# Optimization experiments

Measured on AMD Instinct MI355X. Metric: run time of the kernel, lower is better.

The kernel has to match this reference:

```python
import jax, jax.numpy as jnp
import numpy as np

DIM = 3072
KV_DIM = 2048
HEADS = 16
DIM_HEAD = 128
INNER = HEADS * DIM_HEAD  # 2048
EPS = 1e-5


def layer_norm(x, g, b):
    mu = jnp.mean(x, axis=-1, keepdims=True)
    var = jnp.var(x, axis=-1, keepdims=True)
    return (x - mu) * jax.lax.rsqrt(var + EPS) * g + b


def setup_inputs() -> dict:
    key = jax.random.key(0)
    ks = jax.random.split(key, 8)
    b, n1, n2 = 2, 2048, 2048
    x = jax.random.normal(ks[0], (b, n1, KV_DIM), dtype=jnp.float32)
    latents = jax.random.normal(ks[1], (b, n2, DIM), dtype=jnp.float32)
    w_q = jax.random.normal(ks[2], (DIM, INNER), dtype=jnp.float32) / np.sqrt(DIM)
    w_kv = jax.random.normal(ks[3], (KV_DIM, 2 * INNER), dtype=jnp.float32) / np.sqrt(KV_DIM)
    w_out = jax.random.normal(ks[4], (INNER, DIM), dtype=jnp.float32) / np.sqrt(INNER)
    ln1_g = jnp.ones((KV_DIM,), jnp.float32)
    ln1_b = jnp.zeros((KV_DIM,), jnp.float32)
    ln2_g = jnp.ones((DIM,), jnp.float32)
    ln2_b = jnp.zeros((DIM,), jnp.float32)
    return {"x": x, "latents": latents, "w_q": w_q, "w_kv": w_kv,
            "w_out": w_out, "ln1_g": ln1_g, "ln1_b": ln1_b,
            "ln2_g": ln2_g, "ln2_b": ln2_b}


def reference(x, latents, w_q, w_kv, w_out, ln1_g, ln1_b, ln2_g, ln2_b):
    b, n2, _ = latents.shape
    xn = layer_norm(x, ln1_g, ln1_b)            # (b, n1, kv_dim)
    ln = layer_norm(latents, ln2_g, ln2_b)      # (b, n2, dim)
    q = ln @ w_q                                # (b, n2, inner)
    kv = xn @ w_kv                              # (b, n1, 2*inner)
    k, v = jnp.split(kv, 2, axis=-1)
    # (b, h, n, d)
    def split_heads(t):
        bs, n, _ = t.shape
        return t.reshape(bs, n, HEADS, DIM_HEAD).transpose(0, 2, 1, 3)
    q, k, v = split_heads(q), split_heads(k), split_heads(v)
    scale = 1.0 / np.sqrt(np.sqrt(DIM_HEAD)).astype(np.float32)
    w = jnp.einsum('bhqd,bhkd->bhqk', q * scale, k * scale)
    w = jax.nn.softmax(w.astype(jnp.float32), axis=-1).astype(q.dtype)
    out = jnp.einsum('bhqk,bhkd->bhqd', w, v)
    out = out.transpose(0, 2, 1, 3).reshape(b, n2, INNER)
    return out @ w_out
```

## Files before the change

### kernel.cpp

```cpp
#include <hip/hip_runtime.h>
#include <type_traits>


using u16 = unsigned short;
using u32 = unsigned int;
typedef __attribute__((ext_vector_type(8))) short short8;
typedef __attribute__((ext_vector_type(4))) float floatx4;

typedef __attribute__((address_space(1))) const unsigned int gu32;
typedef __attribute__((address_space(3))) unsigned int lu32;

__device__ __forceinline__ void gld16(void* lds, const void* g) {
  __builtin_amdgcn_global_load_lds((gu32*)g, (lu32*)lds, 16, 0, 0);
}

__device__ inline u16 f2bf(float f) {
  u32 u = __float_as_uint(f);
  u32 r = (u + 0x7FFFu + ((u >> 16) & 1u)) >> 16;
  return (u16)r;
}

template <int L>
__global__ __launch_bounds__(256) void ln_cast(const float* __restrict__ in,
                                               const float* __restrict__ gw,
                                               const float* __restrict__ bw,
                                               u16* __restrict__ out) {
  constexpr int C4 = L / 1024;
  const int row = blockIdx.x;
  const int t = threadIdx.x;
  const float* rp = in + (size_t)row * L;
  float4 v[C4];
  float s = 0.f, ss = 0.f;
#pragma unroll
  for (int c = 0; c < C4; ++c) {
    v[c] = *(const float4*)(rp + (c * 256 + t) * 4);
    s += v[c].x + v[c].y + v[c].z + v[c].w;
    ss += v[c].x * v[c].x + v[c].y * v[c].y + v[c].z * v[c].z + v[c].w * v[c].w;
  }
#pragma unroll
  for (int off = 32; off > 0; off >>= 1) {
    s += __shfl_down(s, off);
    ss += __shfl_down(ss, off);
  }
  __shared__ float red[8];
  const int wave = t >> 6, lane = t & 63;
  if (lane == 0) { red[wave] = s; red[4 + wave] = ss; }
  __syncthreads();
  const float tot = red[0] + red[1] + red[2] + red[3];
  const float tss = red[4] + red[5] + red[6] + red[7];
  const float mu = tot * (1.f / L);
  const float rstd = rsqrtf(tss * (1.f / L) - mu * mu + 1e-5f);
  u16* op = out + (size_t)row * L;
#pragma unroll
  for (int c = 0; c < C4; ++c) {
    const int base = (c * 256 + t) * 4;
    float4 gv = *(const float4*)(gw + base);
    float4 bv = *(const float4*)(bw + base);
    u32 p0 = (u32)f2bf((v[c].x - mu) * rstd * gv.x + bv.x) |
             ((u32)f2bf((v[c].y - mu) * rstd * gv.y + bv.y) << 16);
    u32 p1 = (u32)f2bf((v[c].z - mu) * rstd * gv.z + bv.z) |
             ((u32)f2bf((v[c].w - mu) * rstd * gv.w + bv.w) << 16);
    uint2 pk; pk.x = p0; pk.y = p1;
    *(uint2*)(op + base) = pk;
  }
}

__global__ __launch_bounds__(256) void transpose_cast(const float* __restrict__ in,
                                                      u16* __restrict__ out,
                                                      int R, int C) {
  __shared__ u16 tile[32][33];
  const int c0 = blockIdx.x * 32, r0 = blockIdx.y * 32;
  const int x = threadIdx.x, y = threadIdx.y;
#pragma unroll
  for (int j = 0; j < 4; ++j)
    tile[y + 8 * j][x] = f2bf(in[(size_t)(r0 + y + 8 * j) * C + c0 + x]);
  __syncthreads();
#pragma unroll
  for (int j = 0; j < 4; ++j)
    out[(size_t)(c0 + y + 8 * j) * R + r0 + x] = tile[x][y + 8 * j];
}

__global__ __launch_bounds__(256) void transpose_v(const u16* __restrict__ kvb,
                                                   u16* __restrict__ vT) {
  __shared__ u16 tile[32][33];
  const int bh = blockIdx.z, b = bh >> 4, h = bh & 15;
  const u16* src = kvb + (size_t)b * 2048 * 4096 + 2048 + h * 128;
  u16* dst = vT + (size_t)bh * 128 * 2048;
  const int d0 = blockIdx.x * 32, n0 = blockIdx.y * 32;
  const int x = threadIdx.x, y = threadIdx.y;
#pragma unroll
  for (int j = 0; j < 4; ++j)
    tile[y + 8 * j][x] = src[(size_t)(n0 + y + 8 * j) * 4096 + d0 + x];
  __syncthreads();
#pragma unroll
  for (int j = 0; j < 4; ++j)
    dst[(size_t)(d0 + y + 8 * j) * 2048 + n0 + x] = tile[x][y + 8 * j];
}

template <typename OutT>
__global__ __launch_bounds__(256) void gemm_bt(const u16* __restrict__ A,
                                               const u16* __restrict__ Bt,
                                               OutT* __restrict__ C,
                                               int M, int N, int K) {
  __shared__ u16 As[128 * 32];
  __shared__ u16 Bs[128 * 32];
  const int tid = threadIdx.x;
  const int wave = tid >> 6, lane = tid & 63, l16 = lane & 15, quad = lane >> 4;
  const int wm = (wave >> 1) * 64, wn = (wave & 1) * 64;
  const long m0 = (long)blockIdx.y * 128, n0 = (long)blockIdx.x * 128;
  const int srow = tid >> 2;
  const int sdb = (tid & 3) ^ ((tid >> 3) & 3);
  const u16* Ag0 = A + (m0 + srow) * (long)K + sdb * 8;
  const u16* Bg0 = Bt + (n0 + srow) * (long)K + sdb * 8;
  u16* Al0 = &As[tid * 8];       u16* Al1 = &As[(tid + 256) * 8];
  u16* Bl0 = &Bs[tid * 8];       u16* Bl1 = &Bs[(tid + 256) * 8];
  const long rowoff = 64L * K;

  const floatx4 fz = {0.f, 0.f, 0.f, 0.f};
  floatx4 acc[4][4];
#pragma unroll
  for (int i = 0; i < 4; ++i)
#pragma unroll
    for (int j = 0; j < 4; ++j) acc[i][j] = fz;

  const int sw = (quad ^ ((l16 >> 1) & 3)) * 8;

  for (int k0 = 0; k0 < K; k0 += 32) {
    __syncthreads();
    gld16(Al0, Ag0 + k0);
    gld16(Al1, Ag0 + rowoff + k0);
    gld16(Bl0, Bg0 + k0);
    gld16(Bl1, Bg0 + rowoff + k0);
    __syncthreads();
    short8 a[4], b[4];
#pragma unroll
    for (int i = 0; i < 4; ++i) a[i] = *(const short8*)&As[(wm + i * 16 + l16) * 32 + sw];
#pragma unroll
    for (int j = 0; j < 4; ++j) b[j] = *(const short8*)&Bs[(wn + j * 16 + l16) * 32 + sw];
#pragma unroll
    for (int i = 0; i < 4; ++i)
#pragma unroll
      for (int j = 0; j < 4; ++j)
        acc[i][j] = __builtin_amdgcn_mfma_f32_16x16x32_bf16(a[i], b[j], acc[i][j], 0, 0, 0);
  }

#pragma unroll
  for (int i = 0; i < 4; ++i)
#pragma unroll
    for (int r = 0; r < 4; ++r) {
      const long row = m0 + wm + i * 16 + quad * 4 + r;
#pragma unroll
      for (int j = 0; j < 4; ++j) {
        const long col = n0 + wn + j * 16 + l16;
        if constexpr (std::is_same<OutT, float>::value)
          C[row * N + col] = acc[i][j][r];
        else
          C[row * N + col] = f2bf(acc[i][j][r]);
      }
    }
}

__global__ __launch_bounds__(256, 2) void flash_attn(const u16* __restrict__ Q,
                                                     const u16* __restrict__ KV,
                                                     const u16* __restrict__ VT,
                                                     u16* __restrict__ O) {
  __shared__ u16 Ks[64 * 128];
  __shared__ u16 Vs[128 * 64];
  __shared__ u16 Ps[4][32 * 64];
  const int tid = threadIdx.x;
  const int wave = tid >> 6, lane = tid & 63, l16 = lane & 15, quad = lane >> 4;
  const int bh = blockIdx.y, b = bh >> 4, h = bh & 15;
  const u16* Qb = Q + (size_t)b * 2048 * 2048 + h * 128;
  const u16* Kb = KV + (size_t)b * 2048 * 4096 + h * 128;
  const u16* Vb = VT + (size_t)bh * 128 * 2048;
  u16* Ob = O + (size_t)b * 2048 * 2048 + h * 128;
  const int q0 = blockIdx.x * 128 + wave * 32;

  short8 qf[2][4];
#pragma unroll
  for (int t = 0; t < 2; ++t)
#pragma unroll
    for (int kd = 0; kd < 4; ++kd)
      qf[t][kd] = *(const short8*)&Qb[(size_t)(q0 + t * 16 + l16) * 2048 + kd * 32 + quad * 8];

  short8 onesf;
  {
    union { short8 s; u32 w[4]; } uo;
    const u32 o = (l16 == 0) ? 0x3F803F80u : 0u;
#pragma unroll
    for (int i = 0; i < 4; ++i) uo.w[i] = o;
    onesf = uo.s;
  }

  const floatx4 fz = {0.f, 0.f, 0.f, 0.f};
  floatx4 oacc[2][9];
  float m[2][4];
#pragma unroll
  for (int t = 0; t < 2; ++t) {
#pragma unroll
    for (int jd = 0; jd < 9; ++jd) oacc[t][jd] = fz;
#pragma unroll
    for (int r = 0; r < 4; ++r) m[t][r] = -1e30f;
  }

  u16* Psw = Ps[wave];
  const float sc = 0.08838834764831845f;

  for (int kt = 0; kt < 32; ++kt) {
    const int kv0 = kt * 64;
    __syncthreads();
#pragma unroll
    for (int c = 0; c < 4; ++c) {
      const int li = c * 256 + tid;
      const int krow = li >> 4, kdb = (li & 15) ^ (krow & 15);
      gld16(&Ks[li * 8], Kb + (size_t)(kv0 + krow) * 4096 + kdb * 8);
      const int vrow = li >> 3, vdb = (li & 7) ^ (vrow & 7);
      gld16(&Vs[li * 8], Vb + (size_t)vrow * 2048 + kv0 + vdb * 8);
    }
    __syncthreads();

    floatx4 sacc[2][4];
#pragma unroll
    for (int t = 0; t < 2; ++t)
#pragma unroll
      for (int jn = 0; jn < 4; ++jn) sacc[t][jn] = fz;
#pragma unroll
    for (int jn = 0; jn < 4; ++jn)
#pragma unroll
      for (int kd = 0; kd < 4; ++kd) {
        short8 kb = *(const short8*)&Ks[(jn * 16 + l16) * 128 + ((4 * kd + quad) ^ l16) * 8];
        sacc[0][jn] = __builtin_amdgcn_mfma_f32_16x16x32_bf16(qf[0][kd], kb, sacc[0][jn], 0, 0, 0);
        sacc[1][jn] = __builtin_amdgcn_mfma_f32_16x16x32_bf16(qf[1][kd], kb, sacc[1][jn], 0, 0, 0);
      }

#pragma unroll
    for (int t = 0; t < 2; ++t) {
#pragma unroll
      for (int r = 0; r < 4; ++r) {
        float mx = fmaxf(fmaxf(sacc[t][0][r], sacc[t][1][r]),
                         fmaxf(sacc[t][2][r], sacc[t][3][r]));
#pragma unroll
        for (int off = 8; off > 0; off >>= 1) mx = fmaxf(mx, __shfl_xor(mx, off, 16));
        const float mnew = fmaxf(m[t][r], sc * mx);
        const float alpha = __expf(m[t][r] - mnew);
        m[t][r] = mnew;
        const int q = t * 16 + quad * 4 + r;
        const int mask = (q & 7) ^ (q >> 3);
        u16* prow = &Psw[q * 64 + (l16 & 7)];
#pragma unroll
        for (int jn = 0; jn < 4; ++jn) {
          const float p = __expf(sc * sacc[t][jn][r] - mnew);
          const int slot = (2 * jn + (l16 >> 3)) ^ mask;
          prow[slot * 8] = f2bf(p);
        }
#pragma unroll
        for (int jd = 0; jd < 9; ++jd) oacc[t][jd][r] *= alpha;
      }
    }

    const int pmask0 = (l16 & 7) ^ (l16 >> 3);
    const int pmask1 = (l16 & 7) ^ (2 + (l16 >> 3));
#pragma unroll
    for (int kk = 0; kk < 2; ++kk) {
      const int chunk = 4 * kk + quad;
      short8 pf0 = *(const short8*)&Psw[(l16) * 64 + (chunk ^ pmask0) * 8];
      short8 pf1 = *(const short8*)&Psw[(16 + l16) * 64 + (chunk ^ pmask1) * 8];
#pragma unroll
      for (int jd = 0; jd < 8; ++jd) {
        short8 vb = *(const short8*)&Vs[(jd * 16 + l16) * 64 + (chunk ^ (l16 & 7)) * 8];
        oacc[0][jd] = __builtin_amdgcn_mfma_f32_16x16x32_bf16(pf0, vb, oacc[0][jd], 0, 0, 0);
        oacc[1][jd] = __builtin_amdgcn_mfma_f32_16x16x32_bf16(pf1, vb, oacc[1][jd], 0, 0, 0);
      }
      oacc[0][8] = __builtin_amdgcn_mfma_f32_16x16x32_bf16(pf0, onesf, oacc[0][8], 0, 0, 0);
      oacc[1][8] = __builtin_amdgcn_mfma_f32_16x16x32_bf16(pf1, onesf, oacc[1][8], 0, 0, 0);
    }
  }

#pragma unroll
  for (int t = 0; t < 2; ++t)
#pragma unroll
    for (int r = 0; r < 4; ++r) {
      const float l = __shfl(oacc[t][8][r], lane & 48);
      const float inv = 1.f / l;
      const size_t row = q0 + t * 16 + quad * 4 + r;
#pragma unroll
      for (int jd = 0; jd < 8; ++jd)
        Ob[row * 2048 + jd * 16 + l16] = f2bf(oacc[t][jd][r] * inv);
    }
}

extern "C" void kernel_launch(void* const* d_in, const int* in_sizes, int n_in,
                              void* d_out, int out_size, void* d_ws, size_t ws_size,
                              hipStream_t stream) {
  const float* x       = (const float*)d_in[0];
  const float* latents = (const float*)d_in[1];
  const float* w_q     = (const float*)d_in[2];
  const float* w_kv    = (const float*)d_in[3];
  const float* w_out   = (const float*)d_in[4];
  const float* ln1_g   = (const float*)d_in[5];
  const float* ln1_b   = (const float*)d_in[6];
  const float* ln2_g   = (const float*)d_in[7];
  const float* ln2_b   = (const float*)d_in[8];

  char* ws = (char*)d_ws;
  u16* xn    = (u16*)(ws);
  u16* lnl   = (u16*)(ws + 16777216);
  u16* wqT   = (u16*)(ws + 41943040);
  u16* wkvT  = (u16*)(ws + 54525952);
  u16* woutT = (u16*)(ws + 71303168);
  u16* qb    = (u16*)(ws + 83886080);
  u16* kvb   = (u16*)(ws + 100663296);
  u16* vTb   = lnl;
  u16* attn  = xn;

  ln_cast<2048><<<dim3(4096), 256, 0, stream>>>(x, ln1_g, ln1_b, xn);
  ln_cast<3072><<<dim3(4096), 256, 0, stream>>>(latents, ln2_g, ln2_b, lnl);

  transpose_cast<<<dim3(64, 96), dim3(32, 8), 0, stream>>>(w_q, wqT, 3072, 2048);
  transpose_cast<<<dim3(128, 64), dim3(32, 8), 0, stream>>>(w_kv, wkvT, 2048, 4096);
  transpose_cast<<<dim3(96, 64), dim3(32, 8), 0, stream>>>(w_out, woutT, 2048, 3072);

  gemm_bt<u16><<<dim3(16, 32), 256, 0, stream>>>(lnl, wqT, qb, 4096, 2048, 3072);
  gemm_bt<u16><<<dim3(32, 32), 256, 0, stream>>>(xn, wkvT, kvb, 4096, 4096, 2048);

  transpose_v<<<dim3(4, 64, 32), dim3(32, 8), 0, stream>>>(kvb, vTb);

  flash_attn<<<dim3(16, 32), 256, 0, stream>>>(qb, kvb, vTb, attn);

  gemm_bt<float><<<dim3(24, 32), 256, 0, stream>>>(attn, woutT, (float*)d_out, 4096, 3072, 2048);
}
```

Measured before the change: 617.5 us.

## Double-buffer flash-attention K/V tiles and widen the GEMM K-tile to 64

In flash attention, K and V tiles are now double-buffered in LDS. The next tile's global-to-LDS loads are issued before the current tile is processed, so memory latency can overlap with MFMA and softmax work. The grid becomes 1D with a block remap that groups head blocks, which should improve cache locality. Softmax now uses exp2 with log2(e) folded into the scale. Separately, the bf16 GEMM stages 64-wide K tiles with an 8-way XOR swizzle, halving the number of barrier pairs per output tile. The cost is higher LDS use (about 80KB per attention block) and more register pressure, which could limit occupancy.

```diff
diff --git a/kernel.cpp b/kernel.cpp
--- a/kernel.cpp
+++ b/kernel.cpp
@@ -102,19 +102,17 @@
                                                const u16* __restrict__ Bt,
                                                OutT* __restrict__ C,
                                                int M, int N, int K) {
-  __shared__ u16 As[128 * 32];
-  __shared__ u16 Bs[128 * 32];
+  __shared__ u16 As[128 * 64];
+  __shared__ u16 Bs[128 * 64];
   const int tid = threadIdx.x;
   const int wave = tid >> 6, lane = tid & 63, l16 = lane & 15, quad = lane >> 4;
   const int wm = (wave >> 1) * 64, wn = (wave & 1) * 64;
   const long m0 = (long)blockIdx.y * 128, n0 = (long)blockIdx.x * 128;
-  const int srow = tid >> 2;
-  const int sdb = (tid & 3) ^ ((tid >> 3) & 3);
-  const u16* Ag0 = A + (m0 + srow) * (long)K + sdb * 8;
-  const u16* Bg0 = Bt + (n0 + srow) * (long)K + sdb * 8;
-  u16* Al0 = &As[tid * 8];       u16* Al1 = &As[(tid + 256) * 8];
-  u16* Bl0 = &Bs[tid * 8];       u16* Bl1 = &Bs[(tid + 256) * 8];
-  const long rowoff = 64L * K;
+  const int srow = tid >> 3;
+  const int gc = ((tid & 7) ^ ((tid >> 3) & 7)) * 8;
+  const u16* Ag0 = A + (m0 + srow) * (long)K + gc;
+  const u16* Bg0 = Bt + (n0 + srow) * (long)K + gc;
+  const long rowoff = 32L * K;
 
   const floatx4 fz = {0.f, 0.f, 0.f, 0.f};
   floatx4 acc[4][4];
@@ -123,25 +121,28 @@
 #pragma unroll
     for (int j = 0; j < 4; ++j) acc[i][j] = fz;
 
-  const int sw = (quad ^ ((l16 >> 1) & 3)) * 8;
-
-  for (int k0 = 0; k0 < K; k0 += 32) {
+  for (int k0 = 0; k0 < K; k0 += 64) {
     __syncthreads();
-    gld16(Al0, Ag0 + k0);
-    gld16(Al1, Ag0 + rowoff + k0);
-    gld16(Bl0, Bg0 + k0);
-    gld16(Bl1, Bg0 + rowoff + k0);
+#pragma unroll
+    for (int c = 0; c < 4; ++c) {
+      gld16(&As[(c * 256 + tid) * 8], Ag0 + c * rowoff + k0);
+      gld16(&Bs[(c * 256 + tid) * 8], Bg0 + c * rowoff + k0);
+    }
     __syncthreads();
-    short8 a[4], b[4];
-#pragma unroll
-    for (int i = 0; i < 4; ++i) a[i] = *(const short8*)&As[(wm + i * 16 + l16) * 32 + sw];
-#pragma unroll
-    for (int j = 0; j < 4; ++j) b[j] = *(const short8*)&Bs[(wn + j * 16 + l16) * 32 + sw];
-#pragma unroll
-    for (int i = 0; i < 4; ++i)
-#pragma unroll
-      for (int j = 0; j < 4; ++j)
-        acc[i][j] = __builtin_amdgcn_mfma_f32_16x16x32_bf16(a[i], b[j], acc[i][j], 0, 0, 0);
+#pragma unroll
+    for (int kd = 0; kd < 2; ++kd) {
+      const int sw = ((4 * kd + quad) ^ (l16 & 7)) * 8;
+      short8 a[4], b[4];
+#pragma unroll
+      for (int i = 0; i < 4; ++i) a[i] = *(const short8*)&As[(wm + i * 16 + l16) * 64 + sw];
+#pragma unroll
+      for (int j = 0; j < 4; ++j) b[j] = *(const short8*)&Bs[(wn + j * 16 + l16) * 64 + sw];
+#pragma unroll
+      for (int i = 0; i < 4; ++i)
+#pragma unroll
+        for (int j = 0; j < 4; ++j)
+          acc[i][j] = __builtin_amdgcn_mfma_f32_16x16x32_bf16(a[i], b[j], acc[i][j], 0, 0, 0);
+    }
   }
 
 #pragma unroll
@@ -164,17 +165,20 @@
                                                      const u16* __restrict__ KV,
                                                      const u16* __restrict__ VT,
                                                      u16* __restrict__ O) {
-  __shared__ u16 Ks[64 * 128];
-  __shared__ u16 Vs[128 * 64];
+  __shared__ u16 Ks[2][64 * 128];
+  __shared__ u16 Vs[2][128 * 64];
   __shared__ u16 Ps[4][32 * 64];
   const int tid = threadIdx.x;
   const int wave = tid >> 6, lane = tid & 63, l16 = lane & 15, quad = lane >> 4;
-  const int bh = blockIdx.y, b = bh >> 4, h = bh & 15;
+  const int d = blockIdx.x;
+  const int bh = (d & 7) * 4 + ((d >> 3) & 3);
+  const int qt = d >> 5;
+  const int b = bh >> 4, h = bh & 15;
   const u16* Qb = Q + (size_t)b * 2048 * 2048 + h * 128;
   const u16* Kb = KV + (size_t)b * 2048 * 4096 + h * 128;
   const u16* Vb = VT + (size_t)bh * 128 * 2048;
   u16* Ob = O + (size_t)b * 2048 * 2048 + h * 128;
-  const int q0 = blockIdx.x * 128 + wave * 32;
+  const int q0 = qt * 128 + wave * 32;
 
   short8 qf[2][4];
 #pragma unroll
@@ -204,20 +208,27 @@
   }
 
   u16* Psw = Ps[wave];
-  const float sc = 0.08838834764831845f;
-
-  for (int kt = 0; kt < 32; ++kt) {
-    const int kv0 = kt * 64;
-    __syncthreads();
+  const float sc2 = 0.12751775f;
+
+  auto stage = [&](int buf, int kv0) {
 #pragma unroll
     for (int c = 0; c < 4; ++c) {
       const int li = c * 256 + tid;
       const int krow = li >> 4, kdb = (li & 15) ^ (krow & 15);
-      gld16(&Ks[li * 8], Kb + (size_t)(kv0 + krow) * 4096 + kdb * 8);
+      gld16(&Ks[buf][li * 8], Kb + (size_t)(kv0 + krow) * 4096 + kdb * 8);
       const int vrow = li >> 3, vdb = (li & 7) ^ (vrow & 7);
-      gld16(&Vs[li * 8], Vb + (size_t)vrow * 2048 + kv0 + vdb * 8);
-    }
+      gld16(&Vs[buf][li * 8], Vb + (size_t)vrow * 2048 + kv0 + vdb * 8);
+    }
+  };
+
+  stage(0, 0);
+  int cur = 0;
+
+  for (int kt = 0; kt < 32; ++kt) {
     __syncthreads();
+    if (kt < 31) stage(cur ^ 1, (kt + 1) * 64);
+    const u16* Kc = Ks[cur];
+    const u16* Vc = Vs[cur];
 
     floatx4 sacc[2][4];
 #pragma unroll
@@ -228,7 +239,7 @@
     for (int jn = 0; jn < 4; ++jn)
 #pragma unroll
       for (int kd = 0; kd < 4; ++kd) {
-        short8 kb = *(const short8*)&Ks[(jn * 16 + l16) * 128 + ((4 * kd + quad) ^ l16) * 8];
+        short8 kb = *(const short8*)&Kc[(jn * 16 + l16) * 128 + ((4 * kd + quad) ^ l16) * 8];
         sacc[0][jn] = __builtin_amdgcn_mfma_f32_16x16x32_bf16(qf[0][kd], kb, sacc[0][jn], 0, 0, 0);
         sacc[1][jn] = __builtin_amdgcn_mfma_f32_16x16x32_bf16(qf[1][kd], kb, sacc[1][jn], 0, 0, 0);
       }
@@ -241,15 +252,15 @@
                          fmaxf(sacc[t][2][r], sacc[t][3][r]));
 #pragma unroll
         for (int off = 8; off > 0; off >>= 1) mx = fmaxf(mx, __shfl_xor(mx, off, 16));
-        const float mnew = fmaxf(m[t][r], sc * mx);
-        const float alpha = __expf(m[t][r] - mnew);
+        const float mnew = fmaxf(m[t][r], sc2 * mx);
+        const float alpha = __builtin_amdgcn_exp2f(m[t][r] - mnew);
         m[t][r] = mnew;
         const int q = t * 16 + quad * 4 + r;
         const int mask = (q & 7) ^ (q >> 3);
         u16* prow = &Psw[q * 64 + (l16 & 7)];
 #pragma unroll
         for (int jn = 0; jn < 4; ++jn) {
-          const float p = __expf(sc * sacc[t][jn][r] - mnew);
+          const float p = __builtin_amdgcn_exp2f(fmaf(sc2, sacc[t][jn][r], -mnew));
           const int slot = (2 * jn + (l16 >> 3)) ^ mask;
           prow[slot * 8] = f2bf(p);
         }
@@ -267,13 +278,14 @@
       short8 pf1 = *(const short8*)&Psw[(16 + l16) * 64 + (chunk ^ pmask1) * 8];
 #pragma unroll
       for (int jd = 0; jd < 8; ++jd) {
-        short8 vb = *(const short8*)&Vs[(jd * 16 + l16) * 64 + (chunk ^ (l16 & 7)) * 8];
+        short8 vb = *(const short8*)&Vc[(jd * 16 + l16) * 64 + (chunk ^ (l16 & 7)) * 8];
         oacc[0][jd] = __builtin_amdgcn_mfma_f32_16x16x32_bf16(pf0, vb, oacc[0][jd], 0, 0, 0);
         oacc[1][jd] = __builtin_amdgcn_mfma_f32_16x16x32_bf16(pf1, vb, oacc[1][jd], 0, 0, 0);
       }
       oacc[0][8] = __builtin_amdgcn_mfma_f32_16x16x32_bf16(pf0, onesf, oacc[0][8], 0, 0, 0);
       oacc[1][8] = __builtin_amdgcn_mfma_f32_16x16x32_bf16(pf1, onesf, oacc[1][8], 0, 0, 0);
     }
+    cur ^= 1;
   }
 
 #pragma unroll
@@ -325,7 +337,7 @@
 
   transpose_v<<<dim3(4, 64, 32), dim3(32, 8), 0, stream>>>(kvb, vTb);
 
-  flash_attn<<<dim3(16, 32), 256, 0, stream>>>(qb, kvb, vTb, attn);
+  flash_attn<<<dim3(512), 256, 0, stream>>>(qb, kvb, vTb, attn);
 
   gemm_bt<float><<<dim3(24, 32), 256, 0, stream>>>(attn, woutT, (float*)d_out, 4096, 3072, 2048);
 }
```

After: 572.6 us. -7.3%, faster.
